# Kernel optimization log

Measured on AMD Instinct MI355X. Metric: run time of the kernel, lower is better.

## Reference

```python
import jax, jax.numpy as jnp
import numpy as np

B, S, SR, SN = 8, 1024, 256, 1024
D1 = 768; D2 = 512; D3 = 768; MVH = 256
H = 12; HDC = 32; HDR = 32; HD = 64
MLP_DIM = 3072
LN_EPS = 1e-6

def _ln(x, w):
    mu = jnp.mean(x, axis=-1, keepdims=True)
    var = jnp.var(x, axis=-1, keepdims=True)
    return (x - mu) * jax.lax.rsqrt(var + LN_EPS) * w

def _rope(x, freqs):
    # x: [B,H,S,dr]; freqs: [S, dr//2] (learned RoPE param)
    emb = jnp.concatenate([freqs, freqs], axis=-1)
    cos = jnp.cos(emb); sin = jnp.sin(emb)
    d = x.shape[-1] // 2
    rot = jnp.concatenate([-x[..., d:], x[..., :d]], axis=-1)
    return x * cos + rot * sin

def _rope_freqs(seq, dim, theta=10.0):
    inv_freq = 1.0 / theta ** (np.arange(0, dim, 2, dtype=np.float32) / dim)
    t = np.arange(seq, dtype=np.float32)
    return jnp.asarray(np.outer(t, inv_freq))

def setup_inputs():
    key = jax.random.key(0)
    ks = iter(jax.random.split(key, 48))
    n = lambda shape, s=0.02: jax.random.normal(next(ks), shape, jnp.float32) * s
    return dict(
        input_q=jax.random.normal(next(ks), (B, S, D1), jnp.float32),
        ln_q_w=jnp.ones((D1,), jnp.float32), ln_kv_w=jnp.ones((D1,), jnp.float32),
        Wt_mq=n((SR, S)), Wt_vq=n((SR, S)), Wt_mkv=n((SR, S)), Wt_vkv=n((SR, S)),
        mq_w1=n((D2, D1)), mq_w2=n((MVH, D2)),
        vq_w1=n((D2, D1)), vq_w2=n((MVH, D2)),
        mkv_w1=n((D2, D1)), mkv_w2=n((MVH, D2)),
        vkv_w1=n((D2, D1)), vkv_w2=n((MVH, D2)),
        dirty_zq=n((1, SR, MVH), 1.0), dirty_zkv=n((1, SR, MVH), 1.0),
        e2de=jnp.array([1.0], jnp.float32),
        Wt_qzu=n((SN, SR)), Wt_kzu=n((SN, SR)), Wt_vzu=n((SN, SR)),
        Wt_qr=n((SN, SR)), Wt_kr=n((SN, S)),
        qz_up=n((D2, MVH)), kz_up=n((D2, MVH)), vz_up=n((D2, MVH)),
        q_w=n((H * HDC, D2)), k_w=n((H * HDC, D2)), v_w=n((D3, D2)),
        qr_w=n((H * HDR, MVH)), kr_w=n((H * HDR, D1)),
        rope_q_freqs=_rope_freqs(SN, HDR), rope_k_freqs=_rope_freqs(SN, HDR),
        out_w=n((D3, D3)), ln2_w=jnp.ones((D3,), jnp.float32),
        mlp_w1=n((MLP_DIM, D3)), mlp_w2=n((D3, MLP_DIM)),
        eps_zq=jax.random.normal(next(ks), (B, SR, MVH), jnp.float32),
        eps_zkv=jax.random.normal(next(ks), (B, SR, MVH), jnp.float32),
    )

def reference(input_q, ln_q_w, ln_kv_w, Wt_mq, Wt_vq, Wt_mkv, Wt_vkv, mq_w1, mq_w2, vq_w1, vq_w2, mkv_w1, mkv_w2, vkv_w1, vkv_w2, dirty_zq, dirty_zkv, e2de, Wt_qzu, Wt_kzu, Wt_vzu, Wt_qr, Wt_kr, qz_up, kz_up, vz_up, q_w, k_w, v_w, qr_w, kr_w, rope_q_freqs, rope_k_freqs, out_w, ln2_w, mlp_w1, mlp_w2, eps_zq, eps_zkv):
    lin = lambda x, w: x @ w.T                       # torch Linear: W is [out, in]
    tlin = lambda x, w: jnp.einsum('bsd,rs->brd', x, w)  # Linear along seq axis
    xq = _ln(input_q, ln_q_w)
    xkv = _ln(input_q, ln_kv_w)  # input_kv = input_q (self-attention)
    # latent VAE mean/var: seq compress S->SR then feature D1->D2->MVH
    mean_zq = lin(lin(tlin(xq, Wt_mq), mq_w1), mq_w2)
    var_zq = lin(lin(tlin(xq, Wt_vq), vq_w1), vq_w2)
    mean_zkv = lin(lin(tlin(xkv, Wt_mkv), mkv_w1), mkv_w2)
    var_zkv = lin(lin(tlin(xkv, Wt_vkv), vkv_w1), vkv_w2)
    zq = mean_zq + (e2de * eps_zq + (1.0 - e2de) * dirty_zq) * jnp.exp(0.5 * var_zq)
    zkv = mean_zkv + (e2de * eps_zkv + (1.0 - e2de) * dirty_zkv) * jnp.exp(0.5 * var_zkv)
    # upsample seq SR->SN and features MVH->D2
    qz = lin(tlin(zq, Wt_qzu), qz_up)
    kz = lin(tlin(zkv, Wt_kzu), kz_up)
    vz = lin(tlin(zkv, Wt_vzu), vz_up)
    qr = lin(tlin(zq, Wt_qr), qr_w)        # [B,SN,H*HDR]
    kr = lin(tlin(input_q, Wt_kr), kr_w)   # [B,SN,H*HDR]
    qz = lin(qz, q_w); kz = lin(kz, k_w); vz = lin(vz, v_w)
    heads = lambda t, d: t.reshape(B, SN, H, d).transpose(0, 2, 1, 3)
    q = jnp.concatenate([heads(qz, HDC), _rope(heads(qr, HDR), rope_q_freqs)], axis=-1)
    k = jnp.concatenate([heads(kz, HDC), _rope(heads(kr, HDR), rope_k_freqs)], axis=-1)
    v = heads(vz, HD)
    scores = jnp.einsum('bhqd,bhkd->bhqk', q, k) / jnp.sqrt(jnp.float32(HD))
    o = jnp.einsum('bhqk,bhkd->bhqd', jax.nn.softmax(scores, axis=-1), v)
    o = o.transpose(0, 2, 1, 3).reshape(B, SN, D3)
    x = lin(o, out_w) + input_q
    y = _ln(x, ln2_w)
    y = lin(jax.nn.gelu(lin(y, mlp_w1), approximate=False), mlp_w2)
    return x + y
```

## Files before the change

### kernel.cpp

```cpp
#include <hip/hip_runtime.h>
#include <math.h>

#define B_   8
#define S_   1024
#define SR_  256
#define SN_  1024
#define D1_  768
#define D2_  512
#define D3_  768
#define MVH_ 256
#define H_   12
#define HD_  64
#define MLP_ 3072

typedef __attribute__((ext_vector_type(8))) short bf16x8;
typedef __attribute__((ext_vector_type(4))) float f32x4;

__device__ inline ushort f2bf(float f) {
  uint u = __float_as_uint(f);
  uint r = (u + 0x7fffu + ((u >> 16) & 1u)) >> 16;
  return (ushort)r;
}
__device__ inline float b2f(ushort u) { return __uint_as_float(((uint)u) << 16); }

__device__ inline void gload16(const void* g, void* l) {
  __builtin_amdgcn_global_load_lds(
      (const __attribute__((address_space(1))) void*)g,
      (__attribute__((address_space(3))) void*)l, 16, 0, 0);
}

__device__ inline int xcd_swz(int lin, int n) {
  int xcd = lin & 7, idx = lin >> 3;
  int q = n >> 3, r = n & 7;
  return (xcd < r ? xcd * (q + 1) : r * (q + 1) + (xcd - r) * q) + idx;
}

__global__ __launch_bounds__(256) void ln_dual_b(const float* __restrict__ x,
    const float* __restrict__ w1, const float* __restrict__ w2,
    ushort* __restrict__ o1, ushort* __restrict__ o2, int D) {
  int row = blockIdx.x;
  const float* xr = x + (size_t)row * D;
  int tid = threadIdx.x;
  float s = 0.f, ss = 0.f;
  for (int i = tid; i < D; i += 256) { float v = xr[i]; s += v; ss += v * v; }
  __shared__ float rs[256];
  __shared__ float rq[256];
  rs[tid] = s; rq[tid] = ss;
  __syncthreads();
  for (int off = 128; off > 0; off >>= 1) {
    if (tid < off) { rs[tid] += rs[tid + off]; rq[tid] += rq[tid + off]; }
    __syncthreads();
  }
  float mu  = rs[0] / (float)D;
  float var = rq[0] / (float)D - mu * mu;
  float inv = rsqrtf(var + 1e-6f);
  for (int i = tid; i < D; i += 256) {
    float v = (xr[i] - mu) * inv;
    o1[(size_t)row * D + i] = f2bf(v * w1[i]);
    o2[(size_t)row * D + i] = f2bf(v * w2[i]);
  }
}

__global__ __launch_bounds__(256) void ln_b(const float* __restrict__ x,
    const float* __restrict__ w, ushort* __restrict__ o, int D) {
  int row = blockIdx.x;
  const float* xr = x + (size_t)row * D;
  int tid = threadIdx.x;
  float s = 0.f, ss = 0.f;
  for (int i = tid; i < D; i += 256) { float v = xr[i]; s += v; ss += v * v; }
  __shared__ float rs[256];
  __shared__ float rq[256];
  rs[tid] = s; rq[tid] = ss;
  __syncthreads();
  for (int off = 128; off > 0; off >>= 1) {
    if (tid < off) { rs[tid] += rs[tid + off]; rq[tid] += rq[tid + off]; }
    __syncthreads();
  }
  float mu  = rs[0] / (float)D;
  float var = rq[0] / (float)D - mu * mu;
  float inv = rsqrtf(var + 1e-6f);
  for (int i = tid; i < D; i += 256) {
    float v = (xr[i] - mu) * inv;
    o[(size_t)row * D + i] = f2bf(v * w[i]);
  }
}

__global__ __launch_bounds__(256) void trans_f2b(const float* __restrict__ in,
    ushort* __restrict__ out, int R, int C, long strideEl) {
  __shared__ float tile[32][33];
  int bb = blockIdx.z;
  const float* ib = in + (size_t)bb * strideEl;
  ushort* ob = out + (size_t)bb * strideEl;
  int c0 = blockIdx.x << 5, r0 = blockIdx.y << 5;
  int tx = threadIdx.x & 31, ty = threadIdx.x >> 5;
#pragma unroll
  for (int i = 0; i < 4; ++i)
    tile[ty + 8 * i][tx] = ib[(size_t)(r0 + ty + 8 * i) * C + c0 + tx];
  __syncthreads();
#pragma unroll
  for (int i = 0; i < 4; ++i)
    ob[(size_t)(c0 + ty + 8 * i) * R + r0 + tx] = f2bf(tile[tx][ty + 8 * i]);
}

__global__ __launch_bounds__(256) void trans_b2b(const ushort* __restrict__ in,
    ushort* __restrict__ out, int R, int C, long strideEl) {
  __shared__ ushort tile[32][33];
  int bb = blockIdx.z;
  const ushort* ib = in + (size_t)bb * strideEl;
  ushort* ob = out + (size_t)bb * strideEl;
  int c0 = blockIdx.x << 5, r0 = blockIdx.y << 5;
  int tx = threadIdx.x & 31, ty = threadIdx.x >> 5;
#pragma unroll
  for (int i = 0; i < 4; ++i)
    tile[ty + 8 * i][tx] = ib[(size_t)(r0 + ty + 8 * i) * C + c0 + tx];
  __syncthreads();
#pragma unroll
  for (int i = 0; i < 4; ++i)
    ob[(size_t)(c0 + ty + 8 * i) * R + r0 + tx] = tile[tx][ty + 8 * i];
}

struct ConvTab {
  const float* src[28];
  int off[28];
  int cum[29];
};
__global__ __launch_bounds__(256) void multi_f2b(ConvTab t, ushort* __restrict__ wb,
                                                 int total4) {
  int i = blockIdx.x * 256 + threadIdx.x;
  if (i >= total4) return;
  int ti = 0;
  while (t.cum[ti + 1] <= i) ++ti;
  int j = i - t.cum[ti];
  float4 v = ((const float4*)t.src[ti])[j];
  ushort4 o;
  o.x = f2bf(v.x); o.y = f2bf(v.y); o.z = f2bf(v.z); o.w = f2bf(v.w);
  ((ushort4*)(wb + t.off[ti]))[j] = o;
}

__global__ __launch_bounds__(256) void rope_tab(const float* __restrict__ fq,
    const float* __restrict__ fk, float* __restrict__ ctq, float* __restrict__ stq,
    float* __restrict__ ctk, float* __restrict__ stk, int n) {
  int i = blockIdx.x * 256 + threadIdx.x;
  if (i >= n) return;
  float a = fq[i]; ctq[i] = cosf(a); stq[i] = sinf(a);
  float c = fk[i]; ctk[i] = cosf(c); stk[i] = sinf(c);
}

#define GEMM_BODY(Ab, Bb, STORE)                                                     \
  __shared__ ushort As[128 * 64];                                                    \
  __shared__ ushort Bs[128 * 64];                                                    \
  int tid = threadIdx.x;                                                             \
  int lane = tid & 63, wid = tid >> 6;                                               \
  int m0 = by << 7, n0 = bx << 7;                                                    \
  int wm = (wid >> 1) << 6, wn = (wid & 1) << 6;                                     \
  f32x4 acc[4][4];                                                                   \
  _Pragma("unroll")                                                                  \
  for (int i = 0; i < 4; ++i)                                                        \
    _Pragma("unroll")                                                                \
    for (int j = 0; j < 4; ++j) acc[i][j] = (f32x4){0.f, 0.f, 0.f, 0.f};             \
  char* asb = (char*)As;                                                             \
  char* bsb = (char*)Bs;                                                             \
  int srow = lane >> 3;                                                              \
  int skb  = (lane & 7) << 4;                                                        \
  for (int k0 = 0; k0 < K; k0 += 64) {                                               \
    __syncthreads();                                                                 \
    _Pragma("unroll")                                                                \
    for (int i = 0; i < 4; ++i) {                                                    \
      int rr = wid * 32 + i * 8;                                                     \
      gload16((const char*)Ab + ((size_t)(m0 + rr + srow) * K + k0) * 2 + skb,       \
              asb + rr * 128);                                                       \
      gload16((const char*)Bb + ((size_t)(n0 + rr + srow) * K + k0) * 2 + skb,       \
              bsb + rr * 128);                                                       \
    }                                                                                \
    __syncthreads();                                                                 \
    bf16x8 af[2][4], bf[2][4];                                                       \
    _Pragma("unroll")                                                                \
    for (int h = 0; h < 2; ++h) {                                                    \
      _Pragma("unroll")                                                              \
      for (int m = 0; m < 4; ++m)                                                    \
        af[h][m] = *(bf16x8*)&As[(wm + m * 16 + (lane & 15)) * 64 + h * 32 +         \
                                 ((lane >> 4) << 3)];                                \
      _Pragma("unroll")                                                              \
      for (int n = 0; n < 4; ++n)                                                    \
        bf[h][n] = *(bf16x8*)&Bs[(wn + n * 16 + (lane & 15)) * 64 + h * 32 +         \
                                 ((lane >> 4) << 3)];                                \
    }                                                                                \
    __builtin_amdgcn_s_setprio(1);                                                   \
    _Pragma("unroll")                                                                \
    for (int h = 0; h < 2; ++h)                                                      \
      _Pragma("unroll")                                                              \
      for (int m = 0; m < 4; ++m)                                                    \
        _Pragma("unroll")                                                            \
        for (int n = 0; n < 4; ++n)                                                  \
          acc[m][n] = __builtin_amdgcn_mfma_f32_16x16x32_bf16(af[h][m], bf[h][n],    \
                                                              acc[m][n], 0, 0, 0);   \
    __builtin_amdgcn_s_setprio(0);                                                   \
  }                                                                                  \
  int cr = (lane >> 4) << 2, cc = lane & 15;                                         \
  _Pragma("unroll")                                                                  \
  for (int m = 0; m < 4; ++m)                                                        \
    _Pragma("unroll")                                                                \
    for (int n = 0; n < 4; ++n) {                                                    \
      _Pragma("unroll")                                                              \
      for (int r = 0; r < 4; ++r) {                                                  \
        int row = m0 + wm + m * 16 + cr + r;                                         \
        int col = n0 + wn + n * 16 + cc;                                             \
        float v = acc[m][n][r];                                                      \
        STORE;                                                                       \
      }                                                                              \
    }

template <int EPI>
__global__ __launch_bounds__(256) void gemm_bf16(const ushort* __restrict__ A, long sA,
    const ushort* __restrict__ Bm, long sB, const float* __restrict__ R,
    void* __restrict__ Cout, long sC, int M, int N, int K) {
  int gx = gridDim.x, gy = gridDim.y;
  int nwg = gx * gy * gridDim.z;
  int lin = ((int)blockIdx.z * gy + (int)blockIdx.y) * gx + (int)blockIdx.x;
  lin = xcd_swz(lin, nwg);
  int bx = lin % gx, tt = lin / gx;
  int by = tt % gy, bb = tt / gy;
  const ushort* Ab = A + (size_t)bb * sA;
  const ushort* Bb = Bm + (size_t)bb * sB;
  GEMM_BODY(Ab, Bb,
    if (EPI == 0) {
      ((ushort*)Cout)[(size_t)bb * sC + (size_t)row * N + col] = f2bf(v);
    } else if (EPI == 1) {
      ((float*)Cout)[(size_t)row * N + col] = v + R[(size_t)row * N + col];
    } else {
      float y = 0.7978845608f * (v + 0.044715f * v * v * v);
      float sg = 1.0f / (1.0f + __expf(-2.0f * y));
      ((ushort*)Cout)[(size_t)row * N + col] = f2bf(v * sg);
    })
}

struct GrpTab {
  const ushort* A[32];
  const ushort* Bm[32];
  ushort* C[32];
};
__global__ __launch_bounds__(256) void gemm_grp(GrpTab t, int M, int N, int K) {
  int gx = gridDim.x, gy = gridDim.y;
  int nwg = gx * gy * gridDim.z;
  int lin = ((int)blockIdx.z * gy + (int)blockIdx.y) * gx + (int)blockIdx.x;
  lin = xcd_swz(lin, nwg);
  int bx = lin % gx, tt = lin / gx;
  int by = tt % gy, zz = tt / gy;
  const ushort* Ab = t.A[zz];
  const ushort* Bb = t.Bm[zz];
  ushort* Cb = t.C[zz];
  GEMM_BODY(Ab, Bb, Cb[(size_t)row * N + col] = f2bf(v))
}

__global__ __launch_bounds__(256) void z_combine_b(const ushort* __restrict__ mean,
    const ushort* __restrict__ var, const float* __restrict__ eps,
    const float* __restrict__ dirty, const float* __restrict__ e2de_p,
    ushort* __restrict__ zout, int total, int perBatch) {
  int i = blockIdx.x * 256 + threadIdx.x;
  if (i >= total) return;
  float e = e2de_p[0];
  float v = b2f(mean[i]) +
            (e * eps[i] + (1.0f - e) * dirty[i % perBatch]) * expf(0.5f * b2f(var[i]));
  zout[i] = f2bf(v);
}

__global__ __launch_bounds__(256) void pack_qk_b8(const ushort* __restrict__ zf,
    const ushort* __restrict__ rf, const float* __restrict__ ct,
    const float* __restrict__ st, ushort* __restrict__ out, float scale) {
  int i8 = blockIdx.x * 256 + threadIdx.x;
  int i = i8 << 3;
  int d0 = i & 63;
  int s = (i >> 6) & (S_ - 1);
  int bh = i >> 16;
  int b = bh / H_, h = bh % H_;
  short res[8];
  if (d0 < 32) {
    bf16x8 v = *(const bf16x8*)(zf + ((size_t)(b * S_ + s)) * (H_ * 32) + h * 32 + d0);
#pragma unroll
    for (int j = 0; j < 8; ++j) res[j] = (short)f2bf(b2f((ushort)v[j]) * scale);
  } else {
    const ushort* xr = rf + ((size_t)(b * S_ + s)) * (H_ * 32) + h * 32;
    int dr0 = d0 - 32;
    if (dr0 < 16) {
      bf16x8 xa = *(const bf16x8*)(xr + dr0);
      bf16x8 xb2 = *(const bf16x8*)(xr + dr0 + 16);
#pragma unroll
      for (int j = 0; j < 8; ++j) {
        float c = ct[s * 16 + dr0 + j], sn = st[s * 16 + dr0 + j];
        res[j] = (short)f2bf((b2f((ushort)xa[j]) * c - b2f((ushort)xb2[j]) * sn) * scale);
      }
    } else {
      bf16x8 xa = *(const bf16x8*)(xr + dr0);
      bf16x8 xb2 = *(const bf16x8*)(xr + dr0 - 16);
#pragma unroll
      for (int j = 0; j < 8; ++j) {
        float c = ct[s * 16 + dr0 - 16 + j], sn = st[s * 16 + dr0 - 16 + j];
        res[j] = (short)f2bf((b2f((ushort)xa[j]) * c + b2f((ushort)xb2[j]) * sn) * scale);
      }
    }
  }
  *(bf16x8*)(out + i) = *(bf16x8*)res;
}

__global__ __launch_bounds__(256) void pack_v_b8(const ushort* __restrict__ vzf,
    ushort* __restrict__ out) {
  int i8 = blockIdx.x * 256 + threadIdx.x;
  int i = i8 << 3;
  int d0 = i & 63;
  int s = (i >> 6) & (S_ - 1);
  int bh = i >> 16;
  int b = bh / H_, h = bh % H_;
  bf16x8 v = *(const bf16x8*)(vzf + ((size_t)(b * S_ + s)) * D3_ + h * 64 + d0);
  *(bf16x8*)(out + i) = v;
}

__global__ __launch_bounds__(256) void attn_mfma(const ushort* __restrict__ Q,
    const ushort* __restrict__ K, const ushort* __restrict__ V,
    ushort* __restrict__ O) {
  __shared__ ushort lds[16384];
  char* qc = (char*)lds;
  char* kc = (char*)lds + 8192;
  char* vc = (char*)lds + 16384;
  char* pc = (char*)lds + 24576;
  int tid = threadIdx.x, lane = tid & 63, wid = tid >> 6;
  int nwg = gridDim.x * gridDim.y;
  int lin = (int)blockIdx.y * gridDim.x + (int)blockIdx.x;
  lin = xcd_swz(lin, nwg);
  int qt = lin % gridDim.x;
  int bh = lin / gridDim.x;
  int q0 = qt << 6;
  int b = bh / H_, h = bh % H_;
  const ushort* Qb = Q + ((size_t)bh * S_ + q0) * HD_;
  const ushort* Kb = K + (size_t)bh * S_ * HD_;
  const ushort* Vb = V + (size_t)bh * S_ * HD_;
  {
    int r = tid >> 2, c0 = (tid & 3) * 32;
    const char* src = (const char*)Qb + r * 128;
    uint4 v0 = *(const uint4*)(src + c0);
    uint4 v1 = *(const uint4*)(src + c0 + 16);
    int sw = (r & 7) << 4;
    *(uint4*)(qc + r * 128 + (c0 ^ sw)) = v0;
    *(uint4*)(qc + r * 128 + ((c0 + 16) ^ sw)) = v1;
  }
  __syncthreads();
  bf16x8 aq[2];
  {
    int r = wid * 16 + (lane & 15);
    int sw = (r & 7) << 4;
#pragma unroll
    for (int kk = 0; kk < 2; ++kk) {
      int c2 = kk * 64 + ((lane >> 4) << 4);
      aq[kk] = *(bf16x8*)(qc + r * 128 + (c2 ^ sw));
    }
  }
  f32x4 o_[4];
  float m_[4], l_[4];
#pragma unroll
  for (int i = 0; i < 4; ++i) { o_[i] = (f32x4){0.f,0.f,0.f,0.f}; m_[i] = -1e30f; l_[i] = 0.f; }

  for (int kt = 0; kt < S_ / 64; ++kt) {
    __syncthreads();
    {
      int r = tid >> 2, c0 = (tid & 3) * 32;
      const char* src = (const char*)(Kb + (size_t)(kt * 64 + r) * HD_);
      uint4 v0 = *(const uint4*)(src + c0);
      uint4 v1 = *(const uint4*)(src + c0 + 16);
      int sw = (r & 7) << 4;
      *(uint4*)(kc + r * 128 + (c0 ^ sw)) = v0;
      *(uint4*)(kc + r * 128 + ((c0 + 16) ^ sw)) = v1;
    }
    {
      int kp = tid & 31, g = tid >> 5, d0 = g * 8;
      const ushort* s0 = Vb + (size_t)(kt * 64 + 2 * kp) * HD_ + d0;
      bf16x8 va = *(const bf16x8*)s0;
      bf16x8 vb2 = *(const bf16x8*)(s0 + HD_);
#pragma unroll
      for (int j = 0; j < 8; ++j) {
        int d = d0 + j;
        uint val = (uint)(ushort)va[j] | ((uint)(ushort)vb2[j] << 16);
        *(uint*)(vc + d * 128 + ((kp * 4) ^ ((d & 7) << 4))) = val;
      }
    }
    __syncthreads();
    f32x4 sacc[4];
    __builtin_amdgcn_s_setprio(1);
#pragma unroll
    for (int ksub = 0; ksub < 4; ++ksub) {
      sacc[ksub] = (f32x4){0.f,0.f,0.f,0.f};
#pragma unroll
      for (int kk = 0; kk < 2; ++kk) {
        int r = ksub * 16 + (lane & 15);
        int c2 = kk * 64 + ((lane >> 4) << 4);
        bf16x8 bk = *(bf16x8*)(kc + r * 128 + (c2 ^ ((r & 7) << 4)));
        sacc[ksub] = __builtin_amdgcn_mfma_f32_16x16x32_bf16(aq[kk], bk, sacc[ksub], 0, 0, 0);
      }
    }
    __builtin_amdgcn_s_setprio(0);
    float p[4][4];
#pragma unroll
    for (int rr = 0; rr < 4; ++rr) {
      float cm = fmaxf(fmaxf(sacc[0][rr], sacc[1][rr]), fmaxf(sacc[2][rr], sacc[3][rr]));
      cm = fmaxf(cm, __shfl_xor(cm, 1));
      cm = fmaxf(cm, __shfl_xor(cm, 2));
      cm = fmaxf(cm, __shfl_xor(cm, 4));
      cm = fmaxf(cm, __shfl_xor(cm, 8));
      float mn = fmaxf(m_[rr], cm);
      float al = __expf(m_[rr] - mn);
      float ps = 0.f;
#pragma unroll
      for (int ksub = 0; ksub < 4; ++ksub) {
        float pv = __expf(sacc[ksub][rr] - mn);
        p[ksub][rr] = pv;
        ps += pv;
      }
      ps += __shfl_xor(ps, 1);
      ps += __shfl_xor(ps, 2);
      ps += __shfl_xor(ps, 4);
      ps += __shfl_xor(ps, 8);
      l_[rr] = l_[rr] * al + ps;
      m_[rr] = mn;
#pragma unroll
      for (int ds = 0; ds < 4; ++ds) o_[ds][rr] *= al;
    }
#pragma unroll
    for (int ksub = 0; ksub < 4; ++ksub)
#pragma unroll
      for (int rr = 0; rr < 4; ++rr) {
        int r = wid * 16 + ((lane >> 4) << 2) + rr;
        int cb = (ksub * 16 + (lane & 15)) * 2;
        *(ushort*)(pc + r * 128 + (cb ^ ((r & 7) << 4))) = f2bf(p[ksub][rr]);
      }
    __builtin_amdgcn_s_setprio(1);
#pragma unroll
    for (int kk2 = 0; kk2 < 2; ++kk2) {
      int rA = wid * 16 + (lane & 15);
      int c2 = kk2 * 64 + ((lane >> 4) << 4);
      bf16x8 ap = *(bf16x8*)(pc + rA * 128 + (c2 ^ ((rA & 7) << 4)));
#pragma unroll
      for (int ds = 0; ds < 4; ++ds) {
        int rB = ds * 16 + (lane & 15);
        bf16x8 bv = *(bf16x8*)(vc + rB * 128 + (c2 ^ ((rB & 7) << 4)));
        o_[ds] = __builtin_amdgcn_mfma_f32_16x16x32_bf16(ap, bv, o_[ds], 0, 0, 0);
      }
    }
    __builtin_amdgcn_s_setprio(0);
  }
#pragma unroll
  for (int rr = 0; rr < 4; ++rr) {
    float inv = 1.f / l_[rr];
    int q = q0 + wid * 16 + ((lane >> 4) << 2) + rr;
#pragma unroll
    for (int ds = 0; ds < 4; ++ds) {
      int d = ds * 16 + (lane & 15);
      O[((size_t)(b * S_ + q)) * D3_ + h * HD_ + d] = f2bf(o_[ds][rr] * inv);
    }
  }
}

extern "C" void kernel_launch(void* const* d_in, const int* in_sizes, int n_in,
                              void* d_out, int out_size, void* d_ws, size_t ws_size,
                              hipStream_t stream) {
  const float* input_q = (const float*)d_in[0];
  const float* ln_q_w  = (const float*)d_in[1];
  const float* ln_kv_w = (const float*)d_in[2];
  const float* dirty_zq  = (const float*)d_in[15];
  const float* dirty_zkv = (const float*)d_in[16];
  const float* e2de    = (const float*)d_in[17];
  const float* rope_q_f = (const float*)d_in[31];
  const float* rope_k_f = (const float*)d_in[32];
  const float* ln2_w   = (const float*)d_in[34];
  const float* eps_zq  = (const float*)d_in[37];
  const float* eps_zkv = (const float*)d_in[38];

  ushort* wsu = (ushort*)d_ws;
  ushort* wb    = wsu;
  ushort* xq_b  = wsu + 12124160;
  ushort* xkv_b = wsu + 18415616;
  ushort* xqT   = wsu + 37289984;
  ushort* xkvT  = wsu + 43581440;
  ushort* inT   = wsu + 49872896;
  ushort* t1q   = wsu + 12124160;
  ushort* t1kv  = wsu + 15269888;
  ushort* t2b   = wsu + 24707072;
  ushort* mv    = wsu + 28901376;
  ushort* zqb   = wsu + 30998528;
  ushort* zkvb  = wsu + 31522816;
  ushort* zqT   = wsu + 32047104;
  ushort* zkvT  = wsu + 32571392;
  ushort* up    = wsu + 12124160;
  ushort* vzf   = wsu + 20512768;
  ushort* mid   = wsu + 56164352;
  ushort* tkr   = wsu + 37289984;
  ushort* qzf   = wsu + 68747264;
  ushort* kzf   = wsu + 71892992;
  ushort* qrf   = wsu + 75038720;
  ushort* krf   = wsu + 78184448;
  float*  ctq   = (float*)(wsu + 81330176);
  float*  stq   = ctq + 16384;
  float*  ctk   = ctq + 32768;
  float*  stk   = ctq + 49152;
  ushort* qp    = wsu + 12124160;
  ushort* kp    = wsu + 43581440;
  ushort* vp    = wsu + 49872896;
  ushort* ofb   = wsu + 56164352;
  float*  xb    = (float*)(wsu + 12124160);
  ushort* ylb   = wsu + 37289984;
  ushort* hm    = wsu + 43581440;

  const int W_mq = 0,       W_mkv = 524288;
  const int Wq1 = 1048576,  Wv1 = 1441792,  Wk1 = 1835008,  Wkv1 = 2228224;
  const int Wq2 = 2621440,  Wv2 = 2752512,  Wk2 = 2883584,  Wkv2 = 3014656;
  const int W_qzu = 3145728, W_kzu = 3407872, W_vzu = 3670016, W_qr = 3932160;
  const int W_kr = 4194304, W_qzup = 5242880, W_kzup = 5373952, W_vzup = 5505024;
  const int W_qw = 5636096, W_kw = 5832704,  W_vw = 6029312,  W_qrw = 6422528;
  const int W_krw = 6520832, W_ow = 6815744, W_m1 = 7405568,  W_m2 = 9764864;

  ln_dual_b<<<B_ * S_, 256, 0, stream>>>(input_q, ln_q_w, ln_kv_w, xq_b, xkv_b, D1_);

  {
    dim3 g(D1_ / 32, S_ / 32, B_);
    trans_b2b<<<g, 256, 0, stream>>>(xq_b, xqT, S_, D1_, (long)S_ * D1_);
    trans_b2b<<<g, 256, 0, stream>>>(xkv_b, xkvT, S_, D1_, (long)S_ * D1_);
    trans_f2b<<<g, 256, 0, stream>>>(input_q, inT, S_, D1_, (long)S_ * D1_);
  }

  {
    ConvTab t;
    const int srcIdx[28] = {3,4,5,6, 7,9,11,13, 8,10,12,14, 18,19,20,21, 22,
                            23,24,25, 26,27, 28, 29, 30, 33, 35, 36};
    const int sz[28] = {262144,262144,262144,262144, 393216,393216,393216,393216,
                        131072,131072,131072,131072, 262144,262144,262144,262144,
                        1048576, 131072,131072,131072, 196608,196608, 393216,
                        98304, 294912, 589824, 2359296, 2359296};
    int off = 0, c4 = 0;
    for (int i = 0; i < 28; ++i) {
      t.src[i] = (const float*)d_in[srcIdx[i]];
      t.off[i] = off;
      t.cum[i] = c4;
      off += sz[i];
      c4 += sz[i] / 4;
    }
    t.cum[28] = c4;
    multi_f2b<<<(c4 + 255) / 256, 256, 0, stream>>>(t, wb, c4);
    rope_tab<<<64, 256, 0, stream>>>(rope_q_f, rope_k_f, ctq, stq, ctk, stk, 16384);
  }

  long sXT = (long)S_ * D1_;

  {
    GrpTab t;
    for (int c = 0; c < 2; ++c)
      for (int b = 0; b < 8; ++b) {
        int z = c * 8 + b;
        t.A[z] = wb + (c == 0 ? W_mq : W_mkv);
        t.Bm[z] = (c == 0 ? xqT : xkvT) + (size_t)b * sXT;
        t.C[z] = (c == 0 ? t1q : t1kv) + (size_t)b * 512 * 768;
      }
    dim3 g(D1_ / 128, 512 / 128, 16);
    gemm_grp<<<g, 256, 0, stream>>>(t, 512, D1_, S_);
  }
  {
    GrpTab t;
    const int wo[4] = {Wq1, Wv1, Wk1, Wkv1};
    for (int c = 0; c < 4; ++c)
      for (int b = 0; b < 8; ++b) {
        int z = c * 8 + b;
        ushort* t1 = (c < 2 ? t1q : t1kv);
        t.A[z] = t1 + (size_t)b * 512 * 768 + (size_t)(c & 1) * 256 * 768;
        t.Bm[z] = wb + wo[c];
        t.C[z] = t2b + (size_t)z * 256 * 512;
      }
    dim3 g(D2_ / 128, 256 / 128, 32);
    gemm_grp<<<g, 256, 0, stream>>>(t, 256, D2_, D1_);
  }
  {
    GrpTab t;
    const int wo[4] = {Wq2, Wv2, Wk2, Wkv2};
    for (int c = 0; c < 4; ++c)
      for (int b = 0; b < 8; ++b) {
        int z = c * 8 + b;
        t.A[z] = t2b + (size_t)z * 256 * 512;
        t.Bm[z] = wb + wo[c];
        t.C[z] = mv + (size_t)z * 256 * 256;
      }
    dim3 g(MVH_ / 128, 256 / 128, 32);
    gemm_grp<<<g, 256, 0, stream>>>(t, 256, MVH_, D2_);
  }
  z_combine_b<<<(B_ * SR_ * MVH_) / 256, 256, 0, stream>>>(mv, mv + 8 * 65536,
      eps_zq, dirty_zq, e2de, zqb, B_ * SR_ * MVH_, SR_ * MVH_);
  z_combine_b<<<(B_ * SR_ * MVH_) / 256, 256, 0, stream>>>(mv + 16 * 65536,
      mv + 24 * 65536, eps_zkv, dirty_zkv, e2de, zkvb, B_ * SR_ * MVH_, SR_ * MVH_);
  {
    dim3 g(MVH_ / 32, SR_ / 32, B_);
    trans_b2b<<<g, 256, 0, stream>>>(zqb, zqT, SR_, MVH_, (long)SR_ * MVH_);
    trans_b2b<<<g, 256, 0, stream>>>(zkvb, zkvT, SR_, MVH_, (long)SR_ * MVH_);
  }
  {
    GrpTab t;
    const int wo[4] = {W_qzu, W_kzu, W_vzu, W_qr};
    for (int c = 0; c < 4; ++c)
      for (int b = 0; b < 8; ++b) {
        int z = c * 8 + b;
        t.A[z] = wb + wo[c];
        t.Bm[z] = ((c == 0 || c == 3) ? zqT : zkvT) + (size_t)b * 65536;
        t.C[z] = up + (size_t)z * 1024 * 256;
      }
    dim3 g(MVH_ / 128, SN_ / 128, 32);
    gemm_grp<<<g, 256, 0, stream>>>(t, SN_, MVH_, SR_);
  }
  {
    GrpTab t;
    const int wo[3] = {W_qzup, W_kzup, W_vzup};
    for (int c = 0; c < 3; ++c) {
      t.A[c] = up + (size_t)c * 8 * 1024 * 256;
      t.Bm[c] = wb + wo[c];
      t.C[c] = mid + (size_t)c * 8192 * 512;
    }
    dim3 g(D2_ / 128, (B_ * SN_) / 128, 3);
    gemm_grp<<<g, 256, 0, stream>>>(t, B_ * SN_, D2_, MVH_);
  }
  {
    dim3 g(384 / 128, (B_ * SN_) / 128, 1);
    gemm_bf16<0><<<g, 256, 0, stream>>>(up + (size_t)3 * 8 * 1024 * 256, 0,
        wb + W_qrw, 0, nullptr, qrf, 0, B_ * SN_, 384, MVH_);
  }
  {
    GrpTab t;
    t.A[0] = mid;                      t.Bm[0] = wb + W_qw; t.C[0] = qzf;
    t.A[1] = mid + (size_t)8192 * 512; t.Bm[1] = wb + W_kw; t.C[1] = kzf;
    dim3 g(384 / 128, (B_ * SN_) / 128, 2);
    gemm_grp<<<g, 256, 0, stream>>>(t, B_ * SN_, 384, D2_);
  }
  {
    dim3 g(D3_ / 128, (B_ * SN_) / 128, 1);
    gemm_bf16<0><<<g, 256, 0, stream>>>(mid + (size_t)2 * 8192 * 512, 0,
        wb + W_vw, 0, nullptr, vzf, 0, B_ * SN_, D3_, D2_);
  }
  {
    dim3 g(D1_ / 128, SN_ / 128, B_);
    gemm_bf16<0><<<g, 256, 0, stream>>>(wb + W_kr, 0, inT, sXT, nullptr, tkr,
        (long)SN_ * D1_, SN_, D1_, S_);
  }
  {
    dim3 g(384 / 128, (B_ * SN_) / 128, 1);
    gemm_bf16<0><<<g, 256, 0, stream>>>(tkr, 0, wb + W_krw, 0, nullptr, krf, 0,
        B_ * SN_, 384, D1_);
  }

  int chunks = (B_ * H_ * S_ * HD_) / 8;
  pack_qk_b8<<<chunks / 256, 256, 0, stream>>>(qzf, qrf, ctq, stq, qp, 0.125f);
  pack_qk_b8<<<chunks / 256, 256, 0, stream>>>(kzf, krf, ctk, stk, kp, 1.0f);
  pack_v_b8<<<chunks / 256, 256, 0, stream>>>(vzf, vp);

  {
    dim3 g(S_ / 64, B_ * H_);
    attn_mfma<<<g, 256, 0, stream>>>(qp, kp, vp, ofb);
  }

  {
    dim3 g(D3_ / 128, (B_ * SN_) / 128);
    gemm_bf16<1><<<g, 256, 0, stream>>>(ofb, 0, wb + W_ow, 0, input_q, xb, 0,
                                        B_ * SN_, D3_, D3_);
  }
  ln_b<<<B_ * SN_, 256, 0, stream>>>(xb, ln2_w, ylb, D3_);
  {
    dim3 g(MLP_ / 128, (B_ * SN_) / 128);
    gemm_bf16<2><<<g, 256, 0, stream>>>(ylb, 0, wb + W_m1, 0, nullptr, hm, 0,
                                        B_ * SN_, MLP_, D3_);
  }
  {
    dim3 g(D3_ / 128, (B_ * SN_) / 128);
    gemm_bf16<1><<<g, 256, 0, stream>>>(hm, 0, wb + W_m2, 0, xb, (float*)d_out, 0,
                                        B_ * SN_, D3_, MLP_);
  }
}
```

Baseline: 495.9 us.

## Merge Q/K/V pack kernels, load Q directly, add lazy softmax rescale

The three pack kernels become one launch that picks its section from the block index, which saves two kernel launches. The attention kernel now reads Q fragments straight from global memory into registers instead of staging them through LDS, which removes a sync and shrinks LDS use. The online softmax skips the running-max update and rescale when the new tile max exceeds the current max by at most 8 across the wavefront. This lazy rescaling avoids exp and multiply work, but it lets p values reach up to e^8, so bf16 rounding of P changes slightly.

```diff
diff --git a/kernel.cpp b/kernel.cpp
--- a/kernel.cpp
+++ b/kernel.cpp
@@ -264,15 +264,31 @@
   zout[i] = f2bf(v);
 }
 
-__global__ __launch_bounds__(256) void pack_qk_b8(const ushort* __restrict__ zf,
-    const ushort* __restrict__ rf, const float* __restrict__ ct,
-    const float* __restrict__ st, ushort* __restrict__ out, float scale) {
-  int i8 = blockIdx.x * 256 + threadIdx.x;
+__global__ __launch_bounds__(256) void pack_all(
+    const ushort* __restrict__ qzf, const ushort* __restrict__ qrf,
+    const float* __restrict__ ctq, const float* __restrict__ stq, ushort* __restrict__ qp,
+    const ushort* __restrict__ kzf, const ushort* __restrict__ krf,
+    const float* __restrict__ ctk, const float* __restrict__ stk, ushort* __restrict__ kp,
+    const ushort* __restrict__ vzf, ushort* __restrict__ vp, int nblk) {
+  int sec = blockIdx.x / nblk;
+  int blk = blockIdx.x - sec * nblk;
+  int i8 = blk * 256 + threadIdx.x;
   int i = i8 << 3;
   int d0 = i & 63;
   int s = (i >> 6) & (S_ - 1);
   int bh = i >> 16;
   int b = bh / H_, h = bh % H_;
+  if (sec == 2) {
+    bf16x8 v = *(const bf16x8*)(vzf + ((size_t)(b * S_ + s)) * D3_ + h * 64 + d0);
+    *(bf16x8*)(vp + i) = v;
+    return;
+  }
+  const ushort* zf = (sec == 0) ? qzf : kzf;
+  const ushort* rf = (sec == 0) ? qrf : krf;
+  const float* ct = (sec == 0) ? ctq : ctk;
+  const float* st = (sec == 0) ? stq : stk;
+  ushort* out = (sec == 0) ? qp : kp;
+  float scale = (sec == 0) ? 0.125f : 1.0f;
   short res[8];
   if (d0 < 32) {
     bf16x8 v = *(const bf16x8*)(zf + ((size_t)(b * S_ + s)) * (H_ * 32) + h * 32 + d0);
@@ -302,26 +318,13 @@
   *(bf16x8*)(out + i) = *(bf16x8*)res;
 }
 
-__global__ __launch_bounds__(256) void pack_v_b8(const ushort* __restrict__ vzf,
-    ushort* __restrict__ out) {
-  int i8 = blockIdx.x * 256 + threadIdx.x;
-  int i = i8 << 3;
-  int d0 = i & 63;
-  int s = (i >> 6) & (S_ - 1);
-  int bh = i >> 16;
-  int b = bh / H_, h = bh % H_;
-  bf16x8 v = *(const bf16x8*)(vzf + ((size_t)(b * S_ + s)) * D3_ + h * 64 + d0);
-  *(bf16x8*)(out + i) = v;
-}
-
 __global__ __launch_bounds__(256) void attn_mfma(const ushort* __restrict__ Q,
     const ushort* __restrict__ K, const ushort* __restrict__ V,
     ushort* __restrict__ O) {
-  __shared__ ushort lds[16384];
-  char* qc = (char*)lds;
-  char* kc = (char*)lds + 8192;
-  char* vc = (char*)lds + 16384;
-  char* pc = (char*)lds + 24576;
+  __shared__ ushort lds[12288];
+  char* kc = (char*)lds;
+  char* vc = (char*)lds + 8192;
+  char* pc = (char*)lds + 16384;
   int tid = threadIdx.x, lane = tid & 63, wid = tid >> 6;
   int nwg = gridDim.x * gridDim.y;
   int lin = (int)blockIdx.y * gridDim.x + (int)blockIdx.x;
@@ -333,25 +336,12 @@
   const ushort* Qb = Q + ((size_t)bh * S_ + q0) * HD_;
   const ushort* Kb = K + (size_t)bh * S_ * HD_;
   const ushort* Vb = V + (size_t)bh * S_ * HD_;
-  {
-    int r = tid >> 2, c0 = (tid & 3) * 32;
-    const char* src = (const char*)Qb + r * 128;
-    uint4 v0 = *(const uint4*)(src + c0);
-    uint4 v1 = *(const uint4*)(src + c0 + 16);
-    int sw = (r & 7) << 4;
-    *(uint4*)(qc + r * 128 + (c0 ^ sw)) = v0;
-    *(uint4*)(qc + r * 128 + ((c0 + 16) ^ sw)) = v1;
-  }
-  __syncthreads();
   bf16x8 aq[2];
   {
-    int r = wid * 16 + (lane & 15);
-    int sw = (r & 7) << 4;
-#pragma unroll
-    for (int kk = 0; kk < 2; ++kk) {
-      int c2 = kk * 64 + ((lane >> 4) << 4);
-      aq[kk] = *(bf16x8*)(qc + r * 128 + (c2 ^ sw));
-    }
+    const ushort* qrow = Qb + (size_t)(wid * 16 + (lane & 15)) * HD_;
+#pragma unroll
+    for (int kk = 0; kk < 2; ++kk)
+      aq[kk] = *(const bf16x8*)(qrow + kk * 32 + ((lane >> 4) << 3));
   }
   f32x4 o_[4];
   float m_[4], l_[4];
@@ -404,8 +394,8 @@
       cm = fmaxf(cm, __shfl_xor(cm, 2));
       cm = fmaxf(cm, __shfl_xor(cm, 4));
       cm = fmaxf(cm, __shfl_xor(cm, 8));
-      float mn = fmaxf(m_[rr], cm);
-      float al = __expf(m_[rr] - mn);
+      bool keep = __all(cm - m_[rr] <= 8.0f);
+      float mn = keep ? m_[rr] : fmaxf(m_[rr], cm);
       float ps = 0.f;
 #pragma unroll
       for (int ksub = 0; ksub < 4; ++ksub) {
@@ -417,10 +407,15 @@
       ps += __shfl_xor(ps, 2);
       ps += __shfl_xor(ps, 4);
       ps += __shfl_xor(ps, 8);
-      l_[rr] = l_[rr] * al + ps;
-      m_[rr] = mn;
-#pragma unroll
-      for (int ds = 0; ds < 4; ++ds) o_[ds][rr] *= al;
+      if (keep) {
+        l_[rr] += ps;
+      } else {
+        float al = __expf(m_[rr] - mn);
+        l_[rr] = l_[rr] * al + ps;
+        m_[rr] = mn;
+#pragma unroll
+        for (int ds = 0; ds < 4; ++ds) o_[ds][rr] *= al;
+      }
     }
 #pragma unroll
     for (int ksub = 0; ksub < 4; ++ksub)
@@ -647,10 +642,9 @@
         B_ * SN_, 384, D1_);
   }
 
-  int chunks = (B_ * H_ * S_ * HD_) / 8;
-  pack_qk_b8<<<chunks / 256, 256, 0, stream>>>(qzf, qrf, ctq, stq, qp, 0.125f);
-  pack_qk_b8<<<chunks / 256, 256, 0, stream>>>(kzf, krf, ctk, stk, kp, 1.0f);
-  pack_v_b8<<<chunks / 256, 256, 0, stream>>>(vzf, vp);
+  int nblk = (B_ * H_ * S_ * HD_) / 8 / 256;
+  pack_all<<<3 * nblk, 256, 0, stream>>>(qzf, qrf, ctq, stq, qp,
+                                         kzf, krf, ctk, stk, kp, vzf, vp, nblk);
 
   {
     dim3 g(S_ / 64, B_ * H_);
```

New measurement: 552.5 us. +11.4%, slower.
